# Performance work log

Measured on AMD Instinct MI355X. Metric: run time of the kernel, lower is better.

## Reference

```python
import jax, jax.numpy as jnp
import numpy as np
from jax import lax

B = 8            # IMAGES_PER_GPU
A = 261888       # num_anchors (1024x1024 Mask R-CNN FPN anchors)
PRE_NMS_LIMIT = 6000
PROPOSAL_COUNT = 1000
NMS_THRESHOLD = 0.7


def setup_inputs() -> dict:
    key = jax.random.key(0)
    k1, k2, k3, k4 = jax.random.split(key, 4)
    rpn_probs = jax.random.uniform(k1, (B, A, 2), dtype=jnp.float32)
    rpn_bbox = jax.random.normal(k2, (B, A, 4), dtype=jnp.float32)
    # valid normalized anchors: y1,x1 in [0,0.9], height/width in [0.01,0.1]
    yx = jax.random.uniform(k3, (B, A, 2), minval=0.0, maxval=0.9)
    hw = jax.random.uniform(k4, (B, A, 2), minval=0.01, maxval=0.1)
    anchors = jnp.concatenate([yx, yx + hw], axis=-1)  # (y1, x1, y2, x2)
    return {"rpn_probs": rpn_probs, "rpn_bbox": rpn_bbox, "anchors": anchors}


def _apply_box_deltas(boxes, deltas):
    # boxes, deltas: [..., 4] in (y1, x1, y2, x2) / (dy, dx, log(dh), log(dw))
    h = boxes[..., 2] - boxes[..., 0]
    w = boxes[..., 3] - boxes[..., 1]
    cy = boxes[..., 0] + 0.5 * h + deltas[..., 0] * h
    cx = boxes[..., 1] + 0.5 * w + deltas[..., 1] * w
    h = h * jnp.exp(deltas[..., 2])
    w = w * jnp.exp(deltas[..., 3])
    y1 = cy - 0.5 * h
    x1 = cx - 0.5 * w
    return jnp.stack([y1, x1, y1 + h, x1 + w], axis=-1)


def _nms_single(boxes, scores):
    # boxes: [K, 4] already sorted by score descending; greedy NMS, zero-padded
    areas = (boxes[:, 2] - boxes[:, 0]) * (boxes[:, 3] - boxes[:, 1])

    def step(valid, _):
        idx = jnp.argmax(valid)          # first still-valid = highest score
        has = valid[idx]                 # False when no candidates remain
        box = boxes[idx]
        yy1 = jnp.maximum(box[0], boxes[:, 0])
        xx1 = jnp.maximum(box[1], boxes[:, 1])
        yy2 = jnp.minimum(box[2], boxes[:, 2])
        xx2 = jnp.minimum(box[3], boxes[:, 3])
        inter = jnp.maximum(yy2 - yy1, 0.0) * jnp.maximum(xx2 - xx1, 0.0)
        union = (box[2] - box[0]) * (box[3] - box[1]) + areas - inter
        iou = lax.stop_gradient(jnp.where(union > 0, inter / union, 0.0))
        valid = valid & (iou <= NMS_THRESHOLD)  # also suppresses idx (self IoU = 1)
        return valid, jnp.where(has, box, jnp.zeros_like(box))

    _, selected = lax.scan(step, jnp.ones(boxes.shape[0], dtype=bool), None,
                           length=PROPOSAL_COUNT)
    return selected  # [PROPOSAL_COUNT, 4], zero-padded like tf.pad in original


def reference(rpn_probs, rpn_bbox, anchors):
    std = jnp.asarray([0.1, 0.1, 0.2, 0.2], dtype=rpn_bbox.dtype)  # RPN_BBOX_STD_DEV
    scores = rpn_probs[:, :, 1]                 # fg prob [B, A]
    deltas = rpn_bbox * std
    k = min(PRE_NMS_LIMIT, anchors.shape[1])
    top_scores, ix = lax.top_k(scores, k)       # sorted descending, [B, K]
    idx = ix[..., None]
    deltas_k = jnp.take_along_axis(deltas, idx, axis=1)    # [B, K, 4]
    anchors_k = jnp.take_along_axis(anchors, idx, axis=1)  # [B, K, 4]
    boxes = jnp.clip(_apply_box_deltas(anchors_k, deltas_k), 0.0, 1.0)  # window [0,0,1,1]
    return jax.vmap(_nms_single)(boxes, top_scores)  # [B, PROPOSAL_COUNT, 4]
```

## Files before the change

### kernel.cpp

```cpp
#include <hip/hip_runtime.h>
#include <math.h>
#include <stdint.h>

typedef uint32_t u32; typedef uint64_t u64; typedef uint16_t u16; typedef int32_t i32;

#define BATCH 8
#define NA    261888
#define SEGS  32
#define SEGCHUNK 8184
#define WCHUNK 2046
#define SUBCAP 64
#define NSUB  128
#define TOPK  6000
#define PROP  1000
#define TOP1  1024
#define TMPCAP 2048
#define CACHEB 8192
#define FBMAX 16384
#define MW32  32
#define MBLK  64
#define PSTATIC 0x3F7C0000u

#define OFF_FBK   0
#define OFF_CACHE 1048576
#define OFF_CNT   1572864
#define OFF_STAT  1576960
#define OFF_DONE  1577088
#define OFF_BOX   1577216
#define OFF_AREA  1708288
#define OFF_MASK  1741056
#define WS_NEEDED 2789632


__device__ __forceinline__ void decode_box(const float4 an, const float4 dl,
                                           float4& bx, float& ar) {
    float d0 = __fmul_rn(dl.x, 0.1f), d1 = __fmul_rn(dl.y, 0.1f);
    float d2 = __fmul_rn(dl.z, 0.2f), d3 = __fmul_rn(dl.w, 0.2f);
    float h = __fsub_rn(an.z, an.x), w = __fsub_rn(an.w, an.y);
    float cy = __fadd_rn(__fadd_rn(an.x, __fmul_rn(0.5f, h)), __fmul_rn(d0, h));
    float cx = __fadd_rn(__fadd_rn(an.y, __fmul_rn(0.5f, w)), __fmul_rn(d1, w));
    float h2 = __fmul_rn(h, (float)exp((double)d2));
    float w2 = __fmul_rn(w, (float)exp((double)d3));
    float y1 = __fsub_rn(cy, __fmul_rn(0.5f, h2));
    float x1 = __fsub_rn(cx, __fmul_rn(0.5f, w2));
    float y2 = __fadd_rn(y1, h2);
    float x2 = __fadd_rn(x1, w2);
    y1 = fminf(fmaxf(y1, 0.f), 1.f); x1 = fminf(fmaxf(x1, 0.f), 1.f);
    y2 = fminf(fmaxf(y2, 0.f), 1.f); x2 = fminf(fmaxf(x2, 0.f), 1.f);
    bx = make_float4(y1, x1, y2, x2);
    ar = __fmul_rn(__fsub_rn(y2, y1), __fsub_rn(x2, x1));
}

__device__ __forceinline__ bool sup_pred(const float4 bi, const float ai,
                                         const float4 bj, const float aj) {
    const double tmid = (double)0.7f + 0x1p-25;
    float yy1 = fmaxf(bi.x, bj.x), xx1 = fmaxf(bi.y, bj.y);
    float yy2 = fminf(bi.z, bj.z), xx2 = fminf(bi.w, bj.w);
    float ih = fmaxf(__fsub_rn(yy2, yy1), 0.f);
    float iw = fmaxf(__fsub_rn(xx2, xx1), 0.f);
    float inter = __fmul_rn(ih, iw);
    float uni = __fsub_rn(__fadd_rn(ai, aj), inter);
    return (uni > 0.f) && ((double)inter >= tmid * (double)uni);
}

__global__ __launch_bounds__(256) void k_histcache(const float4* __restrict__ p4,
                                                   u64* __restrict__ cache,
                                                   u32* __restrict__ cnt,
                                                   u32* __restrict__ done) {
    const int b = blockIdx.y, seg = blockIdx.x;
    const int wave = threadIdx.x >> 6, lane = threadIdx.x & 63;
    if (seg == 0 && b == 0 && threadIdx.x < BATCH) done[threadIdx.x] = 0;
    const u64 lmask = (1ull << lane) - 1ull;
    const size_t fbase = ((size_t)b * NA + seg * SEGCHUNK + wave * WCHUNK) >> 1;
    const u32 abase = (u32)(seg * SEGCHUNK + wave * WCHUNK);
    u64* cseg = cache + (size_t)b * CACHEB + (seg * 4 + wave) * SUBCAP;
    u32 wOff = 0;
    #pragma unroll 4
    for (int it = 0; it < 16; ++it) {
        int f = it * 64 + lane;
        bool ok = f < (WCHUNK / 2);
        u32 bitsA = 0, bitsB = 0;
        if (ok) {
            float4 v = p4[fbase + f];
            bitsA = __float_as_uint(v.y);
            bitsB = __float_as_uint(v.w);
        }
        bool pA = ok && bitsA >= PSTATIC;
        bool pB = ok && bitsB >= PSTATIC;
        u64 mA = __ballot(pA);
        u64 mB = __ballot(pB);
        u32 cA = (u32)__popcll(mA);
        if (pA) {
            u32 slot = wOff + (u32)__popcll(mA & lmask);
            if (slot < SUBCAP) cseg[slot] = ((u64)(~bitsA) << 32) | (u64)(abase + 2 * f);
        }
        if (pB) {
            u32 slot = wOff + cA + (u32)__popcll(mB & lmask);
            if (slot < SUBCAP) cseg[slot] = ((u64)(~bitsB) << 32) | (u64)(abase + 2 * f + 1);
        }
        wOff += cA + (u32)__popcll(mB);
    }
    if (lane == 0) cnt[b * NSUB + seg * 4 + wave] = wOff;
}

__global__ __launch_bounds__(1024) void k_sortdec(const u64* __restrict__ cache,
                                                  const u32* __restrict__ cnt,
                                                  const float4* __restrict__ anchors,
                                                  const float4* __restrict__ bbox,
                                                  u32* __restrict__ stat_g,
                                                  float4* __restrict__ boxes,
                                                  float* __restrict__ areas) {
    __shared__ u32 hist[4096];
    __shared__ u32 suffix[4096];
    __shared__ u32 ps[256];
    __shared__ u32 psS[257];
    __shared__ u64 tmp[TMPCAP];
    __shared__ u32 scnt[NSUB];
    __shared__ u32 wq[4];
    __shared__ u32 sP, sN, sBin, stat;
    const int b = blockIdx.x;
    const int tid = threadIdx.x;
    const int lane = tid & 63, wv = tid >> 6;
    if (tid == 0) { stat = 1u; sBin = 0xFFFFFFFFu; }
    for (int i = tid; i < 4096; i += 1024) hist[i] = 0;
    __syncthreads();
    if (tid < NSUB) {
        u32 raw = cnt[b * NSUB + tid];
        scnt[tid] = raw > SUBCAP ? SUBCAP : raw;
        if (raw > SUBCAP) stat = 0u;
    }
    __syncthreads();
    for (int t = tid; t < CACHEB; t += 1024) {
        int sub = t >> 6, off = t & (SUBCAP - 1);
        if (off < (int)scnt[sub]) {
            u32 bits = ~((u32)(cache[(size_t)b * CACHEB + t] >> 32));
            atomicAdd(&hist[(bits >> 6) & 0xFFFu], 1u);
        }
    }
    __syncthreads();
    if (tid < 256) {
        u32 su = 0;
        #pragma unroll
        for (int k = 0; k < 16; ++k) su += hist[tid * 16 + k];
        ps[tid] = su;
    }
    __syncthreads();
    {
        u32 v = (tid < 256) ? ps[tid] : 0u;
        #pragma unroll
        for (int d = 1; d < 64; d <<= 1) {
            u32 o = __shfl_down(v, d);
            if (lane + d < 64) v += o;
        }
        if (tid < 256 && lane == 0) wq[wv] = v;
        __syncthreads();
        if (tid < 256) {
            u32 add = 0;
            for (int q = wv + 1; q < 4; ++q) add += wq[q];
            psS[tid] = v + add;
        }
        if (tid == 0) psS[256] = 0u;
        __syncthreads();
    }
    {
        const int t4 = tid * 4;
        const int seg = tid >> 2;
        const int segEnd = seg * 16 + 15;
        u32 tail = 0;
        for (int bb = t4 + 4; bb <= segEnd; ++bb) tail += hist[bb];
        u32 h0 = hist[t4], h1 = hist[t4 + 1], h2 = hist[t4 + 2], h3 = hist[t4 + 3];
        u32 s3 = psS[seg + 1] + tail;
        u32 s2 = s3 + h3;
        u32 s1 = s2 + h2;
        u32 s0 = s1 + h1;
        suffix[t4] = s0; suffix[t4 + 1] = s1; suffix[t4 + 2] = s2; suffix[t4 + 3] = s3;
        if (s0 < TOP1 && s0 + h0 >= TOP1) sBin = (u32)t4;
        if (s1 < TOP1 && s1 + h1 >= TOP1) sBin = (u32)(t4 + 1);
        if (s2 < TOP1 && s2 + h2 >= TOP1) sBin = (u32)(t4 + 2);
        if (s3 < TOP1 && s3 + h3 >= TOP1) sBin = (u32)(t4 + 3);
    }
    __syncthreads();
    if (tid == 0) {
        if (sBin == 0xFFFFFFFFu) stat = 0u;
        else {
            sP = PSTATIC + (sBin << 6);
            u32 n = suffix[sBin] + hist[sBin];
            sN = n;
            if (n > TMPCAP) stat = 0u;
        }
    }
    __syncthreads();
    if (stat) {
        for (int i = tid; i < 4096; i += 1024) hist[i] = 0;
        __syncthreads();
        const u32 P = sP;
        for (int t = tid; t < CACHEB; t += 1024) {
            int sub = t >> 6, off = t & (SUBCAP - 1);
            if (off < (int)scnt[sub]) {
                u64 key = cache[(size_t)b * CACHEB + t];
                u32 bits = ~((u32)(key >> 32));
                if (bits >= P) {
                    u32 bin = (bits >> 6) & 0xFFFu;
                    u32 arr = atomicAdd(&hist[bin], 1u);
                    tmp[suffix[bin] + arr] = key;
                }
            }
        }
        __syncthreads();
        const u32 n = sN;
        for (u32 t = (u32)tid; t < n; t += 1024) {
            u64 key = tmp[t];
            u32 bits = ~((u32)(key >> 32));
            u32 bin = (bits >> 6) & 0xFFFu;
            u32 base = suffix[bin], len = hist[bin];
            u32 pos = base;
            for (u32 q = base; q < base + len; ++q) pos += (tmp[q] < key) ? 1u : 0u;
            if (pos < TOP1) {
                u32 idx = (u32)key;
                float4 bx; float ar;
                decode_box(anchors[(size_t)b * NA + idx], bbox[(size_t)b * NA + idx], bx, ar);
                boxes[b * TOP1 + pos] = bx;
                areas[b * TOP1 + pos] = ar;
            }
        }
    }
    if (tid == 0) stat_g[b] = stat;
}

__global__ __launch_bounds__(1024) void k_masknms(const float4* __restrict__ boxes,
                                                  const float* __restrict__ areas,
                                                  const float2* __restrict__ p2,
                                                  const float4* __restrict__ bbox,
                                                  const float4* __restrict__ anchors,
                                                  const u32* __restrict__ stat_g,
                                                  u32* __restrict__ done,
                                                  u32* __restrict__ mt_all,
                                                  u64* __restrict__ fbkeys,
                                                  float4* __restrict__ out) {
    __shared__ u32 valid[MW32];
    __shared__ u32 wpre[MW32 + 1];
    __shared__ u32 sWin;
    const int b = blockIdx.y;
    const int tid = threadIdx.x;
    const int wave = tid >> 6, lane = tid & 63;
    u32* mt = mt_all + (size_t)b * MW32 * TOP1;
    {
        const int irow = blockIdx.x * 16 + wave;
        float4 bi = boxes[b * TOP1 + irow];
        float  ai = areas[b * TOP1 + irow];
        u32 myw = 0;
        #pragma unroll
        for (int c = 0; c < 16; ++c) {
            float4 bj = boxes[b * TOP1 + c * 64 + lane];
            float  aj = areas[b * TOP1 + c * 64 + lane];
            u64 word = __ballot(sup_pred(bi, ai, bj, aj));
            if (lane == 2 * c)     myw = (u32)word;
            if (lane == 2 * c + 1) myw = (u32)(word >> 32);
        }
        if (lane < MW32) mt[lane * TOP1 + irow] = myw;
    }
    __syncthreads();
    if (tid == 0) {
        __threadfence();
        u32 old = atomicAdd(&done[b], 1u);
        sWin = (old == (u32)(MBLK - 1)) ? 1u : 0u;
    }
    __syncthreads();
    if (!sWin) return;
    __threadfence();
    const int i = tid;
    const int wv = i >> 6;
    const int lne = i & 63;
    const int wi = i >> 5;
    const u32 bitm = (1u << (i & 31)) - 1u;
    u32 row[MW32];
    #pragma unroll
    for (int w = 0; w < MW32; ++w) {
        u32 v = mt[w * TOP1 + i];
        row[w] = (w < wi) ? v : ((w == wi) ? (v & bitm) : 0u);
    }
    if (i < MW32) valid[i] = 0xFFFFFFFFu;
    __syncthreads();
    bool conv = false;
    for (int it = 0; it < 48; ++it) {
        u32 sup = 0;
        #pragma unroll
        for (int w = 0; w < MW32; ++w) sup |= valid[w] & row[w];
        u64 nb = __ballot(sup == 0u);
        u32 lo = (u32)nb, hi = (u32)(nb >> 32);
        int changed = 0;
        if (lne == 0) changed = (valid[2 * wv] != lo) | (valid[2 * wv + 1] != hi);
        __syncthreads();
        if (lne == 0) { valid[2 * wv] = lo; valid[2 * wv + 1] = hi; }
        if (!__syncthreads_or(changed)) { conv = true; break; }
    }
    __syncthreads();
    if (i == 0) {
        u32 r = 0;
        for (int w = 0; w < MW32; ++w) { wpre[w] = r; r += __popc(valid[w]); }
        wpre[MW32] = r;
    }
    __syncthreads();
    u32 V = wpre[MW32];
    if (conv && V >= PROP && stat_g[b] != 0u) {
        u32 vw = valid[wi];
        bool isv = ((vw >> (i & 31)) & 1u) != 0;
        u32 rank = wpre[wi] + __popc(vw & bitm);
        if (isv && rank < PROP) out[b * PROP + rank] = boxes[b * TOP1 + i];
        return;
    }
    __shared__ float4 abox[PROP];
    __shared__ float  aar[PROP];
    __shared__ u32 fh[4096];
    __shared__ u32 fps[256];
    __shared__ u32 nsh, sP6;
    if (i == 0) nsh = 0;
    for (int z = i; z < 4096; z += 1024) fh[z] = 0;
    __syncthreads();
    for (int a = i; a < NA; a += 1024) {
        u32 bits = __float_as_uint(p2[(size_t)b * NA + a].y);
        atomicAdd(&fh[bits >> 18], 1u);
    }
    __syncthreads();
    if (i < 256) {
        u32 su = 0;
        for (int k = 0; k < 16; ++k) su += fh[i * 16 + k];
        fps[i] = su;
    }
    __syncthreads();
    if (i == 0) {
        u32 acc = 0; int seg = 0;
        for (int t = 255; t >= 0; --t) { if (acc + fps[t] >= TOPK) { seg = t; break; } acc += fps[t]; }
        int b6 = seg * 16; u32 g6 = acc;
        for (int k = 15; k >= 0; --k) {
            u32 c = fh[seg * 16 + k];
            if (g6 + c >= TOPK) { b6 = seg * 16 + k; break; }
            g6 += c;
        }
        sP6 = (u32)b6 << 18;
    }
    __syncthreads();
    u32 P6 = sP6;
    for (int a = i; a < NA; a += 1024) {
        u32 bits = __float_as_uint(p2[(size_t)b * NA + a].y);
        if (bits >= P6) {
            u32 p = atomicAdd(&nsh, 1u);
            if (p < FBMAX) fbkeys[(size_t)b * FBMAX + p] = ((u64)(~bits) << 32) | (u64)a;
        }
    }
    __syncthreads();
    u32 n = nsh; if (n > FBMAX) n = FBMAX;
    volatile u64* vk = (volatile u64*)(fbkeys + (size_t)b * FBMAX);
    for (int i2 = (int)n + i; i2 < FBMAX; i2 += 1024) vk[i2] = ~0ull;
    __syncthreads();
    for (int k = 2; k <= FBMAX; k <<= 1) {
        for (int j = k >> 1; j > 0; j >>= 1) {
            for (int p = i; p < FBMAX / 2; p += 1024) {
                int ii = ((p & ~(j - 1)) << 1) | (p & (j - 1));
                int l = ii | j;
                u64 a = vk[ii], c = vk[l];
                bool up = ((ii & k) == 0);
                if ((a > c) == up) { vk[ii] = c; vk[l] = a; }
            }
            __syncthreads();
        }
    }
    int acc_n = 0;
    int limit = (int)n < TOPK ? (int)n : TOPK;
    for (int t = 0; t < limit && acc_n < PROP; ++t) {
        u32 idx = (u32)vk[t];
        float4 bi2; float ai2;
        decode_box(anchors[(size_t)b * NA + idx], bbox[(size_t)b * NA + idx], bi2, ai2);
        int pred = 0;
        if (i < acc_n) pred = sup_pred(bi2, ai2, abox[i], aar[i]) ? 1 : 0;
        int any = __syncthreads_or(pred);
        if (!any) {
            if (i == 0) {
                abox[acc_n] = bi2; aar[acc_n] = ai2;
                out[b * PROP + acc_n] = bi2;
            }
            ++acc_n;
            __syncthreads();
        }
    }
    for (int t = acc_n + i; t < PROP; t += 1024)
        out[b * PROP + t] = make_float4(0.f, 0.f, 0.f, 0.f);
}


extern "C" void kernel_launch(void* const* d_in, const int* in_sizes, int n_in,
                              void* d_out, int out_size, void* d_ws, size_t ws_size,
                              hipStream_t stream) {
    (void)in_sizes; (void)n_in; (void)out_size;
    if (ws_size < (size_t)WS_NEEDED) return;
    const float2* p2      = (const float2*)d_in[0];
    const float4* p4      = (const float4*)d_in[0];
    const float4* bbox    = (const float4*)d_in[1];
    const float4* anchors = (const float4*)d_in[2];
    float4* out = (float4*)d_out;

    char* ws = (char*)d_ws;
    u64* fbkeys  = (u64*)(ws + OFF_FBK);
    u64* cache   = (u64*)(ws + OFF_CACHE);
    u32* cnt     = (u32*)(ws + OFF_CNT);
    u32* stat_g  = (u32*)(ws + OFF_STAT);
    u32* done    = (u32*)(ws + OFF_DONE);
    float4* boxes= (float4*)(ws + OFF_BOX);
    float* areas = (float*)(ws + OFF_AREA);
    u32* maskT   = (u32*)(ws + OFF_MASK);

    dim3 ghc(SEGS, BATCH), gmn(TOP1 / 16, BATCH);
    k_histcache<<<ghc,   256, 0, stream>>>(p4, cache, cnt, done);
    k_sortdec  <<<BATCH, 1024, 0, stream>>>(cache, cnt, anchors, bbox, stat_g, boxes, areas);
    k_masknms  <<<gmn,  1024, 0, stream>>>(boxes, areas, p2, bbox, anchors, stat_g, done, maskT, fbkeys, out);
}
```

Before: 165.9 us.

## Split mask/NMS kernels, compute only lower-triangular mask, exact blockwise greedy NMS in one wave

The fused mask+NMS kernel and its last-block atomic handoff are replaced by two kernels. The first builds only the lower-triangular IoU suppression mask in 64-bit words using 256-thread blocks. The second resolves greedy NMS chunk by chunk in a single wave, applying suppression from kept earlier chunks and iterating a ballot fixpoint within each chunk. This replaces the block-wide Jacobi iteration with its many __syncthreads, at the cost of an extra launch and a serial single-wave loop.

```diff
diff --git a/kernel.cpp b/kernel.cpp
--- a/kernel.cpp
+++ b/kernel.cpp
@@ -17,15 +17,13 @@
 #define TMPCAP 2048
 #define CACHEB 8192
 #define FBMAX 16384
-#define MW32  32
-#define MBLK  64
+#define NW64  16
 #define PSTATIC 0x3F7C0000u
 
 #define OFF_FBK   0
 #define OFF_CACHE 1048576
 #define OFF_CNT   1572864
 #define OFF_STAT  1576960
-#define OFF_DONE  1577088
 #define OFF_BOX   1577216
 #define OFF_AREA  1708288
 #define OFF_MASK  1741056
@@ -65,11 +63,9 @@
 
 __global__ __launch_bounds__(256) void k_histcache(const float4* __restrict__ p4,
                                                    u64* __restrict__ cache,
-                                                   u32* __restrict__ cnt,
-                                                   u32* __restrict__ done) {
+                                                   u32* __restrict__ cnt) {
     const int b = blockIdx.y, seg = blockIdx.x;
     const int wave = threadIdx.x >> 6, lane = threadIdx.x & 63;
-    if (seg == 0 && b == 0 && threadIdx.x < BATCH) done[threadIdx.x] = 0;
     const u64 lmask = (1ull << lane) - 1ull;
     const size_t fbase = ((size_t)b * NA + seg * SEGCHUNK + wave * WCHUNK) >> 1;
     const u32 abase = (u32)(seg * SEGCHUNK + wave * WCHUNK);
@@ -227,88 +223,83 @@
     if (tid == 0) stat_g[b] = stat;
 }
 
-__global__ __launch_bounds__(1024) void k_masknms(const float4* __restrict__ boxes,
-                                                  const float* __restrict__ areas,
-                                                  const float2* __restrict__ p2,
-                                                  const float4* __restrict__ bbox,
-                                                  const float4* __restrict__ anchors,
-                                                  const u32* __restrict__ stat_g,
-                                                  u32* __restrict__ done,
-                                                  u32* __restrict__ mt_all,
-                                                  u64* __restrict__ fbkeys,
-                                                  float4* __restrict__ out) {
-    __shared__ u32 valid[MW32];
-    __shared__ u32 wpre[MW32 + 1];
-    __shared__ u32 sWin;
+__global__ __launch_bounds__(256) void k_mask(const float4* __restrict__ boxes,
+                                              const float* __restrict__ areas,
+                                              u32* __restrict__ mw32) {
     const int b = blockIdx.y;
+    const int wave = threadIdx.x >> 6, lane = threadIdx.x & 63;
+    const int irow = blockIdx.x * 4 + wave;
+    const int cmax = irow >> 6;
+    u32* mt = mw32 + (size_t)b * (NW64 * TOP1 * 2);
+    float4 bi = boxes[b * TOP1 + irow];
+    float  ai = areas[b * TOP1 + irow];
+    u32 myw = 0;
+    for (int c = 0; c <= cmax; ++c) {
+        float4 bj = boxes[b * TOP1 + c * 64 + lane];
+        float  aj = areas[b * TOP1 + c * 64 + lane];
+        u64 word = __ballot(sup_pred(bi, ai, bj, aj));
+        if (lane == 2 * c)     myw = (u32)word;
+        if (lane == 2 * c + 1) myw = (u32)(word >> 32);
+    }
+    if (lane < 2 * (cmax + 1))
+        mt[((lane >> 1) << 11) + (irow << 1) + (lane & 1)] = myw;
+}
+
+__global__ __launch_bounds__(1024, 4) void k_nms(const u64* __restrict__ mw_all,
+                                                 const float4* __restrict__ boxes,
+                                                 const float2* __restrict__ p2,
+                                                 const float4* __restrict__ bbox,
+                                                 const float4* __restrict__ anchors,
+                                                 const u32* __restrict__ stat_g,
+                                                 u64* __restrict__ fbkeys,
+                                                 float4* __restrict__ out) {
+    __shared__ u64 ldsV[NW64];
+    __shared__ u32 wpre[NW64 + 1];
+    __shared__ u32 sVt;
+    const int b = blockIdx.x;
     const int tid = threadIdx.x;
     const int wave = tid >> 6, lane = tid & 63;
-    u32* mt = mt_all + (size_t)b * MW32 * TOP1;
-    {
-        const int irow = blockIdx.x * 16 + wave;
-        float4 bi = boxes[b * TOP1 + irow];
-        float  ai = areas[b * TOP1 + irow];
-        u32 myw = 0;
+    if (wave == 0) {
+        const u64* mw = mw_all + (size_t)b * (NW64 * TOP1);
+        const u64 lmask = (1ull << lane) - 1ull;
+        u64 V[NW64];
         #pragma unroll
-        for (int c = 0; c < 16; ++c) {
-            float4 bj = boxes[b * TOP1 + c * 64 + lane];
-            float  aj = areas[b * TOP1 + c * 64 + lane];
-            u64 word = __ballot(sup_pred(bi, ai, bj, aj));
-            if (lane == 2 * c)     myw = (u32)word;
-            if (lane == 2 * c + 1) myw = (u32)(word >> 32);
-        }
-        if (lane < MW32) mt[lane * TOP1 + irow] = myw;
-    }
-    __syncthreads();
-    if (tid == 0) {
-        __threadfence();
-        u32 old = atomicAdd(&done[b], 1u);
-        sWin = (old == (u32)(MBLK - 1)) ? 1u : 0u;
-    }
-    __syncthreads();
-    if (!sWin) return;
-    __threadfence();
-    const int i = tid;
-    const int wv = i >> 6;
-    const int lne = i & 63;
-    const int wi = i >> 5;
-    const u32 bitm = (1u << (i & 31)) - 1u;
-    u32 row[MW32];
-    #pragma unroll
-    for (int w = 0; w < MW32; ++w) {
-        u32 v = mt[w * TOP1 + i];
-        row[w] = (w < wi) ? v : ((w == wi) ? (v & bitm) : 0u);
-    }
-    if (i < MW32) valid[i] = 0xFFFFFFFFu;
-    __syncthreads();
-    bool conv = false;
-    for (int it = 0; it < 48; ++it) {
-        u32 sup = 0;
-        #pragma unroll
-        for (int w = 0; w < MW32; ++w) sup |= valid[w] & row[w];
-        u64 nb = __ballot(sup == 0u);
-        u32 lo = (u32)nb, hi = (u32)(nb >> 32);
-        int changed = 0;
-        if (lne == 0) changed = (valid[2 * wv] != lo) | (valid[2 * wv + 1] != hi);
-        __syncthreads();
-        if (lne == 0) { valid[2 * wv] = lo; valid[2 * wv + 1] = hi; }
-        if (!__syncthreads_or(changed)) { conv = true; break; }
-    }
-    __syncthreads();
-    if (i == 0) {
-        u32 r = 0;
-        for (int w = 0; w < MW32; ++w) { wpre[w] = r; r += __popc(valid[w]); }
-        wpre[MW32] = r;
-    }
-    __syncthreads();
-    u32 V = wpre[MW32];
-    if (conv && V >= PROP && stat_g[b] != 0u) {
-        u32 vw = valid[wi];
-        bool isv = ((vw >> (i & 31)) & 1u) != 0;
-        u32 rank = wpre[wi] + __popc(vw & bitm);
+        for (int c = 0; c < NW64; ++c) {
+            const int i = (c << 6) + lane;
+            u64 ext = 0;
+            #pragma unroll
+            for (int w = 0; w < c; ++w)
+                ext |= mw[(w << 10) + i] & V[w];
+            const u64 intern = mw[(c << 10) + i] & lmask;
+            const bool extSup = (ext != 0ull);
+            u64 v = ~0ull;
+            for (int it = 0; it < 64; ++it) {
+                bool alive = (!extSup) && ((intern & v) == 0ull);
+                u64 nv = __ballot(alive);
+                if (nv == v) break;
+                v = nv;
+            }
+            V[c] = v;
+        }
+        if (lane == 0) {
+            u32 r = 0;
+            #pragma unroll
+            for (int c = 0; c < NW64; ++c) { ldsV[c] = V[c]; wpre[c] = r; r += (u32)__popcll(V[c]); }
+            wpre[NW64] = r; sVt = r;
+        }
+    }
+    __syncthreads();
+    const u32 Vt = sVt;
+    if (Vt >= PROP && stat_g[b] != 0u) {
+        const int i = tid;
+        const int w = i >> 6, bit = i & 63;
+        u64 vw = ldsV[w];
+        bool isv = ((vw >> bit) & 1ull) != 0ull;
+        u32 rank = wpre[w] + (u32)__popcll(vw & ((1ull << bit) - 1ull));
         if (isv && rank < PROP) out[b * PROP + rank] = boxes[b * TOP1 + i];
         return;
     }
+    const int i = tid;
     __shared__ float4 abox[PROP];
     __shared__ float  aar[PROP];
     __shared__ u32 fh[4096];
@@ -404,13 +395,14 @@
     u64* cache   = (u64*)(ws + OFF_CACHE);
     u32* cnt     = (u32*)(ws + OFF_CNT);
     u32* stat_g  = (u32*)(ws + OFF_STAT);
-    u32* done    = (u32*)(ws + OFF_DONE);
     float4* boxes= (float4*)(ws + OFF_BOX);
     float* areas = (float*)(ws + OFF_AREA);
-    u32* maskT   = (u32*)(ws + OFF_MASK);
-
-    dim3 ghc(SEGS, BATCH), gmn(TOP1 / 16, BATCH);
-    k_histcache<<<ghc,   256, 0, stream>>>(p4, cache, cnt, done);
+    u32* mw32    = (u32*)(ws + OFF_MASK);
+    u64* mw64    = (u64*)(ws + OFF_MASK);
+
+    dim3 ghc(SEGS, BATCH), gmask(TOP1 / 4, BATCH);
+    k_histcache<<<ghc,   256, 0, stream>>>(p4, cache, cnt);
     k_sortdec  <<<BATCH, 1024, 0, stream>>>(cache, cnt, anchors, bbox, stat_g, boxes, areas);
-    k_masknms  <<<gmn,  1024, 0, stream>>>(boxes, areas, p2, bbox, anchors, stat_g, done, maskT, fbkeys, out);
-}
+    k_mask     <<<gmask, 256, 0, stream>>>(boxes, areas, mw32);
+    k_nms      <<<BATCH, 1024, 0, stream>>>(mw64, boxes, p2, bbox, anchors, stat_g, fbkeys, out);
+}
```

Result: faster. 141.6 us (-14.7%).
